# Kernel optimization log

Hardware: AMD Instinct MI355X
Metric: run time of the kernel (lower is better)

## Reference

```python
import jax, jax.numpy as jnp
import numpy as np

BATCH = 512          # bs_large + bs_small
COMBINED_BS = 320    # bs_large + bs_small // (r_large // r_small)
R = 64               # r_large
K = 4096             # hidden dim, fixed in the TIR kernel
N_ADAPT = 80         # combined adapters


def setup_inputs() -> dict:
    key = jax.random.key(0)
    k1, k2, k3, k4 = jax.random.split(key, 4)
    x = jax.random.normal(k1, (BATCH, 1, K), dtype=jnp.float32)
    xids = jax.random.randint(k2, (COMBINED_BS * R,), 0, BATCH, dtype=jnp.int32)
    wids = jax.random.randint(k3, (COMBINED_BS,), 0, N_ADAPT, dtype=jnp.int32)
    A = jax.random.normal(k4, (N_ADAPT, K, R), dtype=jnp.float32) * 0.02
    return {"x": x, "xids": xids, "wids": wids, "A": A}


def reference(x, xids, wids, A):
    # out[c, 0, r] = sum_k x[xids[c*R + r], 0, k] * A[wids[c], k, r]
    C = wids.shape[0]
    r = A.shape[2]
    tok = xids.reshape(C, r)          # per-output-element token ids
    xg = x[tok, 0, :]                 # (C, R, K) gathered activations
    Ag = A[wids]                      # (C, K, R) gathered adapters
    out = jnp.einsum('crk,ckr->cr', xg, Ag)
    return out[:, None, :]            # (C, 1, R)
```

## Files before the change

### kernel.cpp

```cpp
#include <hip/hip_runtime.h>
#include <stdint.h>

namespace {
constexpr int BATCH  = 512;
constexpr int CBS    = 320;
constexpr int R      = 64;
constexpr int K      = 4096;
constexpr int NADAPT = 80;
constexpr int GRP    = 4;
constexpr int NGRP   = CBS / GRP;
constexpr int SPLIT  = 16;
constexpr int KS     = K / SPLIT;
constexpr int KW     = KS / 4;
constexpr int NT     = 256;

constexpr size_t WS_X_OFF  = 4096;
constexpr size_t WS_NEEDED = WS_X_OFF + (size_t)BATCH * K * 2;

__device__ inline uint16_t f2bf(float f) {
    uint32_t u = __float_as_uint(f);
    u += 0x7fffu + ((u >> 16) & 1u);
    return (uint16_t)(u >> 16);
}
__device__ inline float bflo(uint32_t u) { return __uint_as_float(u << 16); }
__device__ inline float bfhi(uint32_t u) { return __uint_as_float(u & 0xffff0000u); }
}

__global__ __launch_bounds__(256)
void prep(const float* __restrict__ x, uint16_t* __restrict__ xb,
          const int* __restrict__ wids, int* __restrict__ perm,
          float* __restrict__ out, int out_size)
{
    const int bid = blockIdx.x;
    const int t   = threadIdx.x;
    if (bid == 0) {
        __shared__ int hist[NADAPT];
        __shared__ int offs[NADAPT];
        if (t < NADAPT) hist[t] = 0;
        __syncthreads();
        for (int c = t; c < CBS; c += 256) atomicAdd(&hist[wids[c]], 1);
        __syncthreads();
        if (t == 0) {
            int run = 0;
            for (int i = 0; i < NADAPT; ++i) { offs[i] = run; run += hist[i]; }
        }
        __syncthreads();
        for (int c = t; c < CBS; c += 256) {
            const int pos = atomicAdd(&offs[wids[c]], 1);
            perm[pos] = c;
        }
    } else if (bid <= BATCH * K / 1024) {
        const int i = (bid - 1) * 256 + t;
        const float4 v = ((const float4*)x)[i];
        ushort4 o;
        o.x = f2bf(v.x); o.y = f2bf(v.y); o.z = f2bf(v.z); o.w = f2bf(v.w);
        ((ushort4*)xb)[i] = o;
    } else {
        const int i4 = (bid - (1 + BATCH * K / 1024)) * 256 + t;
        const int e  = i4 * 4;
        if (e + 3 < out_size) {
            ((float4*)out)[i4] = make_float4(0.f, 0.f, 0.f, 0.f);
        } else {
            for (int q = e; q < out_size; ++q) out[q] = 0.f;
        }
    }
}

__global__ __launch_bounds__(NT)
void lora_main(const int* __restrict__ xids,
               const int* __restrict__ wids,
               const float* __restrict__ A,
               const uint16_t* __restrict__ xb,
               const int* __restrict__ perm,
               float* __restrict__ out)
{
    const int bid = blockIdx.x;
    const int g   = bid >> 4;
    const int s   = bid & 15;
    const int t   = threadIdx.x;
    const int wv  = t >> 6;
    const int r   = t & 63;
    const int k0  = s * KS + wv * KW;

    const int c0 = perm[GRP * g + 0], c1 = perm[GRP * g + 1],
              c2 = perm[GRP * g + 2], c3 = perm[GRP * g + 3];
    const int w0 = wids[c0], w1 = wids[c1], w2 = wids[c2], w3 = wids[c3];

    const uint16_t* __restrict__ xp0 = xb + (size_t)xids[c0 * R + r] * K + k0;
    const uint16_t* __restrict__ xp1 = xb + (size_t)xids[c1 * R + r] * K + k0;
    const uint16_t* __restrict__ xp2 = xb + (size_t)xids[c2 * R + r] * K + k0;
    const uint16_t* __restrict__ xp3 = xb + (size_t)xids[c3 * R + r] * K + k0;

    const size_t kb = (size_t)k0 * R + r;
    const float* __restrict__ A0 = A + (size_t)w0 * (K * R) + kb;
    const float* __restrict__ A1 = A + (size_t)w1 * (K * R) + kb;
    const float* __restrict__ A2 = A + (size_t)w2 * (K * R) + kb;
    const float* __restrict__ A3 = A + (size_t)w3 * (K * R) + kb;

    float acc0 = 0.f, acc1 = 0.f, acc2 = 0.f, acc3 = 0.f;

#define FMA8(ACC, V, AP) do {                                              \
        ACC = fmaf(bflo((V).x), (AP)[0], ACC);                             \
        ACC = fmaf(bfhi((V).x), (AP)[1], ACC);                             \
        ACC = fmaf(bflo((V).y), (AP)[2], ACC);                             \
        ACC = fmaf(bfhi((V).y), (AP)[3], ACC);                             \
        ACC = fmaf(bflo((V).z), (AP)[4], ACC);                             \
        ACC = fmaf(bfhi((V).z), (AP)[5], ACC);                             \
        ACC = fmaf(bflo((V).w), (AP)[6], ACC);                             \
        ACC = fmaf(bfhi((V).w), (AP)[7], ACC);                             \
    } while (0)

    if (w0 == w3) {
#pragma unroll 2
        for (int kk = 0; kk < KW; kk += 8) {
            const uint4 v0 = *(const uint4*)(xp0 + kk);
            const uint4 v1 = *(const uint4*)(xp1 + kk);
            const uint4 v2 = *(const uint4*)(xp2 + kk);
            const uint4 v3 = *(const uint4*)(xp3 + kk);
            float a[8];
#pragma unroll
            for (int q = 0; q < 8; ++q) a[q] = A0[(size_t)(kk + q) * R];
            FMA8(acc0, v0, a);
            FMA8(acc1, v1, a);
            FMA8(acc2, v2, a);
            FMA8(acc3, v3, a);
        }
    } else {
#pragma unroll 2
        for (int kk = 0; kk < KW; kk += 8) {
            const uint4 v0 = *(const uint4*)(xp0 + kk);
            const uint4 v1 = *(const uint4*)(xp1 + kk);
            const uint4 v2 = *(const uint4*)(xp2 + kk);
            const uint4 v3 = *(const uint4*)(xp3 + kk);
            float a0[8], a1[8], a2[8], a3[8];
#pragma unroll
            for (int q = 0; q < 8; ++q) {
                const size_t o = (size_t)(kk + q) * R;
                a0[q] = A0[o]; a1[q] = A1[o]; a2[q] = A2[o]; a3[q] = A3[o];
            }
            FMA8(acc0, v0, a0);
            FMA8(acc1, v1, a1);
            FMA8(acc2, v2, a2);
            FMA8(acc3, v3, a3);
        }
    }
#undef FMA8

    atomicAdd(&out[c0 * R + r], acc0);
    atomicAdd(&out[c1 * R + r], acc1);
    atomicAdd(&out[c2 * R + r], acc2);
    atomicAdd(&out[c3 * R + r], acc3);
}

__global__ __launch_bounds__(NT)
void lora_fallback(const float* __restrict__ x,
                   const int*   __restrict__ xids,
                   const int*   __restrict__ wids,
                   const float* __restrict__ A,
                   float*       __restrict__ out)
{
    constexpr int FKS = 512, FTK = 64, FNT_TILES = 8, FNW = 4;
    __shared__ float xsf[FTK * R];
    __shared__ float red[FNW * R];
    const int bid  = blockIdx.x;
    const int c    = bid >> 3;
    const int s    = bid & 7;
    const int t    = threadIdx.x;
    const int wave = t >> 6;
    const int lane = t & 63;
    const int r4   = lane & 15;
    const int kq   = lane >> 4;
    const int wid  = wids[c];
    const float* __restrict__ Aw = A + (size_t)wid * (K * R);
    const int rw  = t >> 2;
    const int jq  = t & 3;
    const int tok = xids[c * R + rw];
    const float* __restrict__ xrow = x + (size_t)tok * K + s * FKS + jq * 16;
    float4 acc = make_float4(0.f, 0.f, 0.f, 0.f);
    float4 pv[4];
    {
        const float4* src = (const float4*)xrow;
#pragma unroll
        for (int ii = 0; ii < 4; ++ii) pv[ii] = src[ii];
    }
    for (int tile = 0; tile < FNT_TILES; ++tile) {
#pragma unroll
        for (int ii = 0; ii < 4; ++ii) {
            const int kk = jq * 16 + ii * 4;
            xsf[(kk + 0) * R + rw] = pv[ii].x;
            xsf[(kk + 1) * R + rw] = pv[ii].y;
            xsf[(kk + 2) * R + rw] = pv[ii].z;
            xsf[(kk + 3) * R + rw] = pv[ii].w;
        }
        __syncthreads();
        if (tile + 1 < FNT_TILES) {
            const float4* src = (const float4*)(xrow + (tile + 1) * FTK);
#pragma unroll
            for (int ii = 0; ii < 4; ++ii) pv[ii] = src[ii];
        }
        const int kw = wave * 16 + kq;
        const float* __restrict__ Ap =
            Aw + (size_t)(s * FKS + tile * FTK + kw) * R + 4 * r4;
#pragma unroll
        for (int i = 0; i < 4; ++i) {
            float4 av = *(const float4*)(Ap + (size_t)(4 * i) * R);
            float4 xv = *(const float4*)(&xsf[(kw + 4 * i) * R + 4 * r4]);
            acc.x = fmaf(xv.x, av.x, acc.x);
            acc.y = fmaf(xv.y, av.y, acc.y);
            acc.z = fmaf(xv.z, av.z, acc.z);
            acc.w = fmaf(xv.w, av.w, acc.w);
        }
        __syncthreads();
    }
#pragma unroll
    for (int m = 16; m < 64; m <<= 1) {
        acc.x += __shfl_xor(acc.x, m, 64);
        acc.y += __shfl_xor(acc.y, m, 64);
        acc.z += __shfl_xor(acc.z, m, 64);
        acc.w += __shfl_xor(acc.w, m, 64);
    }
    if (kq == 0) {
        float* rd = &red[wave * R + 4 * r4];
        rd[0] = acc.x; rd[1] = acc.y; rd[2] = acc.z; rd[3] = acc.w;
    }
    __syncthreads();
    if (wave == 0) {
        float sum = red[lane] + red[R + lane] + red[2 * R + lane] + red[3 * R + lane];
        atomicAdd(&out[c * R + lane], sum);
    }
}

extern "C" void kernel_launch(void* const* d_in, const int* in_sizes, int n_in,
                              void* d_out, int out_size, void* d_ws, size_t ws_size,
                              hipStream_t stream)
{
    (void)in_sizes; (void)n_in;
    const float* x    = (const float*)d_in[0];
    const int*   xids = (const int*)d_in[1];
    const int*   wids = (const int*)d_in[2];
    const float* A    = (const float*)d_in[3];
    float* out        = (float*)d_out;

    if (ws_size >= WS_NEEDED) {
        int*      perm = (int*)d_ws;
        uint16_t* xbw  = (uint16_t*)((char*)d_ws + WS_X_OFF);
        const int ncvt = BATCH * K / 1024;
        const int nz   = (out_size + 1023) / 1024;
        hipLaunchKernelGGL(prep, dim3(1 + ncvt + nz), dim3(256), 0, stream,
                           x, xbw, wids, perm, out, out_size);
        hipLaunchKernelGGL(lora_main, dim3(NGRP * SPLIT), dim3(NT), 0, stream,
                           xids, wids, A, xbw, perm, out);
    } else {
        hipMemsetAsync(out, 0, (size_t)out_size * sizeof(float), stream);
        hipLaunchKernelGGL(lora_fallback, dim3(CBS * 8), dim3(NT), 0, stream,
                           x, xids, wids, A, out);
    }
}
```

Before: 179.9 us.

## Stage gathered activations in double-buffered LDS and reduce across waves before atomics

Each wave now loads one combo's gathered bf16 activation row in 32-element tiles into a double-buffered shared-memory array, prefetching the next tile into registers while computing. Every wave then reads all four combos' activations for its own 8-element k slice from LDS and multiplies them with the matching adapter rows. Partial sums are reduced across waves in shared memory, so each thread issues one global atomicAdd instead of four. The change also adds an occupancy hint to launch_bounds, at the price of a __syncthreads per tile and extra LDS traffic.

```diff
diff --git a/kernel.cpp b/kernel.cpp
--- a/kernel.cpp
+++ b/kernel.cpp
@@ -11,7 +11,8 @@
 constexpr int NGRP   = CBS / GRP;
 constexpr int SPLIT  = 16;
 constexpr int KS     = K / SPLIT;
-constexpr int KW     = KS / 4;
+constexpr int TK     = 32;
+constexpr int NTILE  = KS / TK;
 constexpr int NT     = 256;
 
 constexpr size_t WS_X_OFF  = 4096;
@@ -66,7 +67,7 @@
     }
 }
 
-__global__ __launch_bounds__(NT)
+__global__ __launch_bounds__(NT, 4)
 void lora_main(const int* __restrict__ xids,
                const int* __restrict__ wids,
                const float* __restrict__ A,
@@ -74,32 +75,35 @@
                const int* __restrict__ perm,
                float* __restrict__ out)
 {
+    __shared__ __align__(16) uint32_t xs[2][GRP * 1024];
+    __shared__ float red[4 * GRP * 64];
+
     const int bid = blockIdx.x;
     const int g   = bid >> 4;
     const int s   = bid & 15;
     const int t   = threadIdx.x;
     const int wv  = t >> 6;
     const int r   = t & 63;
-    const int k0  = s * KS + wv * KW;
 
     const int c0 = perm[GRP * g + 0], c1 = perm[GRP * g + 1],
               c2 = perm[GRP * g + 2], c3 = perm[GRP * g + 3];
     const int w0 = wids[c0], w1 = wids[c1], w2 = wids[c2], w3 = wids[c3];
 
-    const uint16_t* __restrict__ xp0 = xb + (size_t)xids[c0 * R + r] * K + k0;
-    const uint16_t* __restrict__ xp1 = xb + (size_t)xids[c1 * R + r] * K + k0;
-    const uint16_t* __restrict__ xp2 = xb + (size_t)xids[c2 * R + r] * K + k0;
-    const uint16_t* __restrict__ xp3 = xb + (size_t)xids[c3 * R + r] * K + k0;
-
-    const size_t kb = (size_t)k0 * R + r;
-    const float* __restrict__ A0 = A + (size_t)w0 * (K * R) + kb;
-    const float* __restrict__ A1 = A + (size_t)w1 * (K * R) + kb;
-    const float* __restrict__ A2 = A + (size_t)w2 * (K * R) + kb;
-    const float* __restrict__ A3 = A + (size_t)w3 * (K * R) + kb;
+    const int cc = wv;
+    const int ccombo = (wv == 0) ? c0 : (wv == 1) ? c1 : (wv == 2) ? c2 : c3;
+    const uint16_t* __restrict__ xrow =
+        xb + (size_t)xids[ccombo * R + r] * K + s * KS;
+
+    const size_t koff = (size_t)(s * KS) * R + r;
+    const float* __restrict__ Ab0 = A + (size_t)w0 * (K * R) + koff;
+    const float* __restrict__ Ab1 = A + (size_t)w1 * (K * R) + koff;
+    const float* __restrict__ Ab2 = A + (size_t)w2 * (K * R) + koff;
+    const float* __restrict__ Ab3 = A + (size_t)w3 * (K * R) + koff;
+    const bool uniform = (w0 == w3);
 
     float acc0 = 0.f, acc1 = 0.f, acc2 = 0.f, acc3 = 0.f;
 
-#define FMA8(ACC, V, AP) do {                                              \
+#define DOT8(ACC, V, AP) do {                                              \
         ACC = fmaf(bflo((V).x), (AP)[0], ACC);                             \
         ACC = fmaf(bfhi((V).x), (AP)[1], ACC);                             \
         ACC = fmaf(bflo((V).y), (AP)[2], ACC);                             \
@@ -110,46 +114,85 @@
         ACC = fmaf(bfhi((V).w), (AP)[7], ACC);                             \
     } while (0)
 
-    if (w0 == w3) {
-#pragma unroll 2
-        for (int kk = 0; kk < KW; kk += 8) {
-            const uint4 v0 = *(const uint4*)(xp0 + kk);
-            const uint4 v1 = *(const uint4*)(xp1 + kk);
-            const uint4 v2 = *(const uint4*)(xp2 + kk);
-            const uint4 v3 = *(const uint4*)(xp3 + kk);
+    uint4 p0, p1, p2, p3;
+    {
+        const uint4* src = (const uint4*)xrow;
+        p0 = src[0]; p1 = src[1]; p2 = src[2]; p3 = src[3];
+        uint32_t* wb = &xs[0][cc * 1024 + 4 * r];
+        *(uint4*)(wb +   0) = p0;
+        *(uint4*)(wb + 256) = p1;
+        *(uint4*)(wb + 512) = p2;
+        *(uint4*)(wb + 768) = p3;
+    }
+
+    for (int tile = 0; tile < NTILE; ++tile) {
+        if (tile + 1 < NTILE) {
+            const uint4* src = (const uint4*)(xrow + (tile + 1) * TK);
+            p0 = src[0]; p1 = src[1]; p2 = src[2]; p3 = src[3];
+        }
+        __syncthreads();
+
+        const uint32_t* __restrict__ B = &xs[tile & 1][wv * 256 + 4 * r];
+        const size_t ao = (size_t)(tile * TK + wv * 8) * R;
+        const uint4 x0 = *(const uint4*)(B + 0 * 1024);
+        const uint4 x1 = *(const uint4*)(B + 1 * 1024);
+        const uint4 x2 = *(const uint4*)(B + 2 * 1024);
+        const uint4 x3 = *(const uint4*)(B + 3 * 1024);
+
+        if (uniform) {
+            const float* At = Ab0 + ao;
             float a[8];
 #pragma unroll
-            for (int q = 0; q < 8; ++q) a[q] = A0[(size_t)(kk + q) * R];
-            FMA8(acc0, v0, a);
-            FMA8(acc1, v1, a);
-            FMA8(acc2, v2, a);
-            FMA8(acc3, v3, a);
-        }
-    } else {
-#pragma unroll 2
-        for (int kk = 0; kk < KW; kk += 8) {
-            const uint4 v0 = *(const uint4*)(xp0 + kk);
-            const uint4 v1 = *(const uint4*)(xp1 + kk);
-            const uint4 v2 = *(const uint4*)(xp2 + kk);
-            const uint4 v3 = *(const uint4*)(xp3 + kk);
-            float a0[8], a1[8], a2[8], a3[8];
-#pragma unroll
-            for (int q = 0; q < 8; ++q) {
-                const size_t o = (size_t)(kk + q) * R;
-                a0[q] = A0[o]; a1[q] = A1[o]; a2[q] = A2[o]; a3[q] = A3[o];
+            for (int q = 0; q < 8; ++q) a[q] = At[(size_t)q * R];
+            DOT8(acc0, x0, a);
+            DOT8(acc1, x1, a);
+            DOT8(acc2, x2, a);
+            DOT8(acc3, x3, a);
+        } else {
+            {
+                const float* At = Ab0 + ao; float a[8];
+#pragma unroll
+                for (int q = 0; q < 8; ++q) a[q] = At[(size_t)q * R];
+                DOT8(acc0, x0, a);
             }
-            FMA8(acc0, v0, a0);
-            FMA8(acc1, v1, a1);
-            FMA8(acc2, v2, a2);
-            FMA8(acc3, v3, a3);
-        }
-    }
-#undef FMA8
-
-    atomicAdd(&out[c0 * R + r], acc0);
-    atomicAdd(&out[c1 * R + r], acc1);
-    atomicAdd(&out[c2 * R + r], acc2);
-    atomicAdd(&out[c3 * R + r], acc3);
+            {
+                const float* At = Ab1 + ao; float a[8];
+#pragma unroll
+                for (int q = 0; q < 8; ++q) a[q] = At[(size_t)q * R];
+                DOT8(acc1, x1, a);
+            }
+            {
+                const float* At = Ab2 + ao; float a[8];
+#pragma unroll
+                for (int q = 0; q < 8; ++q) a[q] = At[(size_t)q * R];
+                DOT8(acc2, x2, a);
+            }
+            {
+                const float* At = Ab3 + ao; float a[8];
+#pragma unroll
+                for (int q = 0; q < 8; ++q) a[q] = At[(size_t)q * R];
+                DOT8(acc3, x3, a);
+            }
+        }
+
+        if (tile + 1 < NTILE) {
+            uint32_t* wb = &xs[(tile + 1) & 1][cc * 1024 + 4 * r];
+            *(uint4*)(wb +   0) = p0;
+            *(uint4*)(wb + 256) = p1;
+            *(uint4*)(wb + 512) = p2;
+            *(uint4*)(wb + 768) = p3;
+        }
+    }
+#undef DOT8
+
+    red[wv * 256 +   0 + r] = acc0;
+    red[wv * 256 +  64 + r] = acc1;
+    red[wv * 256 + 128 + r] = acc2;
+    red[wv * 256 + 192 + r] = acc3;
+    __syncthreads();
+    const float sum = red[0 * 256 + wv * 64 + r] + red[1 * 256 + wv * 64 + r] +
+                      red[2 * 256 + wv * 64 + r] + red[3 * 256 + wv * 64 + r];
+    atomicAdd(&out[ccombo * R + r], sum);
 }
 
 __global__ __launch_bounds__(NT)
```

New measurement: 160.0 us. -11.1%, faster.
